# Kernel optimization log

Hardware: AMD Instinct MI355X
Metric: run time of the kernel (lower is better)

## Reference

```python
import jax, jax.numpy as jnp
import numpy as np


def gcn_conv(x, W, src, dst, edge_weight, n_nodes):
    """PyG GCNConv (bias=False, add_self_loops=True, normalize=True).
    out = D^{-1/2} (A + I) D^{-1/2} X W, with deg computed from edge weights
    into each destination node plus the self-loop weight 1.
    """
    h = x @ W  # [N, F_out]
    deg = jax.ops.segment_sum(edge_weight, dst, num_segments=n_nodes) + 1.0  # self-loop w=1
    dinv = jax.lax.rsqrt(deg)  # deg >= 1 so safe
    norm = dinv[src] * edge_weight * dinv[dst]  # [E]
    # gather -> weight -> scatter-add
    agg = jax.ops.segment_sum(norm[:, None] * h[src], dst, num_segments=n_nodes)
    # self-loop contribution: norm_ii = deg_i^{-1}
    return agg + h * (1.0 / deg)[:, None]


def setup_inputs() -> dict:
    key = jax.random.key(0)
    k1, k2, k3, k4, k5 = jax.random.split(key, 5)
    N, E = 10000, 160000
    in_ch, hidden, out_ch = 512, 512, 256
    x = jax.random.normal(k1, (N, in_ch), dtype=jnp.float32)
    edge_index = jax.random.randint(k2, (2, E), 0, N, dtype=jnp.int64)
    edge_weight = jax.random.uniform(k3, (E,), dtype=jnp.float32)
    # Glorot-style init like torch_geometric.nn.dense.linear
    W1 = jax.random.normal(k4, (in_ch, hidden), dtype=jnp.float32) * (1.0 / np.sqrt(in_ch))
    W2 = jax.random.normal(k5, (hidden, out_ch), dtype=jnp.float32) * (1.0 / np.sqrt(hidden))
    return {"x": x, "edge_index": edge_index, "edge_weight": edge_weight, "W1": W1, "W2": W2}


def reference(x, edge_index, edge_weight, W1, W2):
    n_nodes = x.shape[0]
    src, dst = edge_index[0], edge_index[1]
    h = jax.nn.relu(gcn_conv(x, W1, src, dst, edge_weight, n_nodes))
    # dropout is identity in eval mode
    return gcn_conv(h, W2, src, dst, edge_weight, n_nodes)
```

## Files before the change

### kernel.cpp

```cpp
#include <hip/hip_runtime.h>

#define N_NODES 10000
#define N_EDGES 160000
#define M_PAD   10112
#define MT      79
#define KT      8
#define ELLW    64

typedef short s8v __attribute__((ext_vector_type(8)));
typedef short s4v __attribute__((ext_vector_type(4)));
typedef float f4v __attribute__((ext_vector_type(4)));

__device__ inline short f2bf(float f) {
    unsigned u = __builtin_bit_cast(unsigned, f);
    u += 0x7FFF + ((u >> 16) & 1);
    return (short)(u >> 16);
}
__device__ inline float bf2f(short s) {
    return __builtin_bit_cast(float, ((unsigned)(unsigned short)s) << 16);
}

#define GLD_LDS16(g, l)                                                      \
    __builtin_amdgcn_global_load_lds(                                        \
        (const __attribute__((address_space(1))) unsigned int*)(g),          \
        (__attribute__((address_space(3))) unsigned int*)(l), 16, 0, 0)

__global__ __launch_bounds__(256) void k_prep(const float* __restrict__ x,
                                              const float* __restrict__ W1,
                                              const float* __restrict__ W2,
                                              char* __restrict__ x_bf,
                                              char* __restrict__ w1T,
                                              char* __restrict__ w2T,
                                              float* __restrict__ deg,
                                              int* __restrict__ count) {
    int bid = blockIdx.x;
    if (bid < 2528) {
        long long t = (long long)bid * 256 + threadIdx.x;
        int gr = (int)(t >> 6);
        int c  = (int)(t & 63);
        s8v v;
        if (gr < N_NODES) {
            const float* p = &x[(long long)gr * 512 + c * 8];
#pragma unroll
            for (int j = 0; j < 8; j++) v[j] = f2bf(p[j]);
        } else {
#pragma unroll
            for (int j = 0; j < 8; j++) v[j] = 0;
        }
        int r = gr & 127, tm = gr >> 7, tk = c >> 3, sc = c & 7;
        int slot = sc ^ (r & 7);
        *(s8v*)&x_bf[(((long long)tm * KT + tk) << 14) + r * 128 + slot * 16] = v;
    } else if (bid < 2720) {
        const float* W;
        char* out;
        int ncols, t;
        if (bid < 2656) { W = W1; out = w1T; ncols = 512; t = (bid - 2528) * 256 + threadIdx.x; }
        else            { W = W2; out = w2T; ncols = 256; t = (bid - 2656) * 256 + threadIdx.x; }
        int n = t >> 6;
        int c = t & 63;
        s8v v;
#pragma unroll
        for (int j = 0; j < 8; j++) v[j] = f2bf(W[(long long)(c * 8 + j) * ncols + n]);
        int r = n & 127, tn = n >> 7, tk = c >> 3, sc = c & 7;
        int slot = sc ^ (r & 7);
        *(s8v*)&out[(((long long)tn * KT + tk) << 14) + r * 128 + slot * 16] = v;
    } else {
        int i = (bid - 2720) * 256 + threadIdx.x;
        if (i < N_NODES) { deg[i] = 1.0f; count[i] = 0; }
    }
}

__device__ __forceinline__ void gemm_block(const char* __restrict__ ga,
                                           const char* __restrict__ gb,
                                           short* __restrict__ Cb,
                                           int M, int N, int row_blk, int col_blk,
                                           char* As, char* Bs) {
    int tid = threadIdx.x, lane = tid & 63, w = tid >> 6;
    int wr = w >> 1, wc = w & 1;

    f4v acc[4][4];
#pragma unroll
    for (int m = 0; m < 4; m++)
#pragma unroll
        for (int n = 0; n < 4; n++) acc[m][n] = (f4v){0.f, 0.f, 0.f, 0.f};

    for (int kt = 0; kt < KT; ++kt) {
        const char* a0 = ga + (kt << 14);
        const char* b0 = gb + (kt << 14);
#pragma unroll
        for (int j = 0; j < 4; ++j) {
            int off = (j * 256 + w * 64) * 16;
            GLD_LDS16(a0 + off + lane * 16, As + off);
            GLD_LDS16(b0 + off + lane * 16, Bs + off);
        }
        __syncthreads();

#pragma unroll
        for (int kk = 0; kk < 2; ++kk) {
            s8v a[4], b[4];
#pragma unroll
            for (int m = 0; m < 4; ++m) {
                int r = wr * 64 + m * 16 + (lane & 15);
                int slot = ((lane >> 4) + kk * 4) ^ (r & 7);
                a[m] = *(const s8v*)&As[r * 128 + slot * 16];
            }
#pragma unroll
            for (int n = 0; n < 4; ++n) {
                int r = wc * 64 + n * 16 + (lane & 15);
                int slot = ((lane >> 4) + kk * 4) ^ (r & 7);
                b[n] = *(const s8v*)&Bs[r * 128 + slot * 16];
            }
#pragma unroll
            for (int m = 0; m < 4; ++m)
#pragma unroll
                for (int n = 0; n < 4; ++n)
                    acc[m][n] = __builtin_amdgcn_mfma_f32_16x16x32_bf16(a[m], b[n], acc[m][n], 0, 0, 0);
        }
        __syncthreads();
    }

    int row0 = row_blk * 128 + wr * 64;
    int col0 = col_blk * 128 + wc * 64;
#pragma unroll
    for (int m = 0; m < 4; ++m) {
#pragma unroll
        for (int q = 0; q < 4; ++q) {
            int row = row0 + m * 16 + (lane >> 4) * 4 + q;
            if (row < M) {
#pragma unroll
                for (int n = 0; n < 4; ++n) {
                    int col = col0 + n * 16 + (lane & 15);
                    Cb[(long long)row * N + col] = f2bf(acc[m][n][q]);
                }
            }
        }
    }
}

__global__ __launch_bounds__(256) void k_gemm1_deg(const char* __restrict__ A,
                                                   const char* __restrict__ B,
                                                   short* __restrict__ Cb,
                                                   const int* __restrict__ src,
                                                   const int* __restrict__ dst,
                                                   const float* __restrict__ wgt,
                                                   float* __restrict__ deg,
                                                   int* __restrict__ count,
                                                   int2* __restrict__ ell) {
    int bid = blockIdx.x;
    if (bid >= 316) {
        int e = (bid - 316) * 256 + threadIdx.x;
        if (e < N_EDGES) {
            int d = dst[e];
            float wv = wgt[e];
            atomicAdd(&deg[d], wv);
            int pos = atomicAdd(&count[d], 1);
            if (pos < ELLW)
                ell[(long long)d * ELLW + pos] = make_int2(src[e], __float_as_int(wv));
        }
        return;
    }
    __shared__ char As[16384];
    __shared__ char Bs[16384];
    int bx = bid & 3, by = bid >> 2;
    gemm_block(A + ((long long)by * KT << 14), B + ((long long)bx * KT << 14),
               Cb, N_NODES, 512, by, bx, As, Bs);
}

__device__ __forceinline__ void xcd_map(int b, int& by, int& bx) {
    by = (b & 7) * 10 + ((b >> 3) >> 2);
    bx = (b >> 3) & 3;
}

__global__ __launch_bounds__(256) void k_gemm2(const char* __restrict__ A,
                                               const char* __restrict__ w2T,
                                               short* __restrict__ Cb) {
    int by, bx;
    xcd_map(blockIdx.x, by, bx);
    if (by >= MT) return;

    __shared__ char As[16384];
    __shared__ char Bs[8192];
    int tid = threadIdx.x, lane = tid & 63, w = tid >> 6;
    int wr = w >> 1, wc = w & 1;

    const char* ga = A + ((long long)by * KT << 14);
    const char* gbase = w2T + ((long long)(bx >> 1) * KT << 14) + (bx & 1) * 8192;

    f4v acc[4][2];
#pragma unroll
    for (int m = 0; m < 4; m++)
#pragma unroll
        for (int n = 0; n < 2; n++) acc[m][n] = (f4v){0.f, 0.f, 0.f, 0.f};

    for (int kt = 0; kt < KT; ++kt) {
        const char* a0 = ga + (kt << 14);
        const char* b0 = gbase + (kt << 14);
#pragma unroll
        for (int j = 0; j < 4; ++j) {
            int off = (j * 256 + w * 64) * 16;
            GLD_LDS16(a0 + off + lane * 16, As + off);
        }
#pragma unroll
        for (int j = 0; j < 2; ++j) {
            int off = (j * 256 + w * 64) * 16;
            GLD_LDS16(b0 + off + lane * 16, Bs + off);
        }
        __syncthreads();

#pragma unroll
        for (int kk = 0; kk < 2; ++kk) {
            s8v a[4], b[2];
#pragma unroll
            for (int m = 0; m < 4; ++m) {
                int r = wr * 64 + m * 16 + (lane & 15);
                int slot = ((lane >> 4) + kk * 4) ^ (r & 7);
                a[m] = *(const s8v*)&As[r * 128 + slot * 16];
            }
#pragma unroll
            for (int n = 0; n < 2; ++n) {
                int r = wc * 32 + n * 16 + (lane & 15);
                int slot = ((lane >> 4) + kk * 4) ^ (r & 7);
                b[n] = *(const s8v*)&Bs[r * 128 + slot * 16];
            }
#pragma unroll
            for (int m = 0; m < 4; ++m)
#pragma unroll
                for (int n = 0; n < 2; ++n)
                    acc[m][n] = __builtin_amdgcn_mfma_f32_16x16x32_bf16(a[m], b[n], acc[m][n], 0, 0, 0);
        }
        __syncthreads();
    }

    int row0 = by * 128 + wr * 64;
    int col0 = bx * 64 + wc * 32;
#pragma unroll
    for (int m = 0; m < 4; ++m) {
#pragma unroll
        for (int q = 0; q < 4; ++q) {
            int row = row0 + m * 16 + (lane >> 4) * 4 + q;
            if (row < N_NODES) {
#pragma unroll
                for (int n = 0; n < 2; ++n) {
                    int col = col0 + n * 16 + (lane & 15);
                    Cb[(long long)row * 256 + col] = f2bf(acc[m][n][q]);
                }
            }
        }
    }
}

template <int F, bool RELU, bool OUT_TILED>
__global__ __launch_bounds__(256) void k_gather(const int2* __restrict__ ell,
                                                const int* __restrict__ count,
                                                const short* __restrict__ hb,
                                                const float* __restrict__ deg,
                                                void* __restrict__ outp,
                                                int n_waves) {
    const int FPT = F / 64;
    int wave = (int)((blockIdx.x * (long long)blockDim.x + threadIdx.x) >> 6);
    if (wave >= n_waves) return;
    int lane = threadIdx.x & 63;

    float acc[FPT];
#pragma unroll
    for (int j = 0; j < FPT; j++) acc[j] = 0.f;

    if (wave < N_NODES) {
        float dg = deg[wave];
        float inv = 1.0f / dg;
        float dinv_d = rsqrtf(dg);
        {
            if constexpr (FPT == 8) {
                s8v v = *(const s8v*)&hb[(long long)wave * F + lane * 8];
#pragma unroll
                for (int j = 0; j < 8; j++) acc[j] = bf2f(v[j]) * inv;
            } else {
                s4v v = *(const s4v*)&hb[(long long)wave * F + lane * 4];
#pragma unroll
                for (int j = 0; j < 4; j++) acc[j] = bf2f(v[j]) * inv;
            }
        }
        int cnt = count[wave];
        if (cnt > ELLW) cnt = ELLW;
        const int2* row = &ell[(long long)wave * ELLW];
        int p = 0;
        for (; p + 7 < cnt; p += 8) {
            int2 e[8];
#pragma unroll
            for (int q = 0; q < 8; q++) e[q] = row[p + q];
            float nn[8];
#pragma unroll
            for (int q = 0; q < 8; q++)
                nn[q] = rsqrtf(deg[e[q].x]) * __int_as_float(e[q].y) * dinv_d;
            if constexpr (FPT == 8) {
                s8v v[8];
#pragma unroll
                for (int q = 0; q < 8; q++)
                    v[q] = *(const s8v*)&hb[(long long)e[q].x * F + lane * 8];
#pragma unroll
                for (int j = 0; j < 8; j++) {
#pragma unroll
                    for (int q = 0; q < 8; q++) acc[j] += nn[q] * bf2f(v[q][j]);
                }
            } else {
                s4v v[8];
#pragma unroll
                for (int q = 0; q < 8; q++)
                    v[q] = *(const s4v*)&hb[(long long)e[q].x * F + lane * 4];
#pragma unroll
                for (int j = 0; j < 4; j++) {
#pragma unroll
                    for (int q = 0; q < 8; q++) acc[j] += nn[q] * bf2f(v[q][j]);
                }
            }
        }
        for (; p + 3 < cnt; p += 4) {
            int2 e0 = row[p], e1 = row[p + 1], e2 = row[p + 2], e3 = row[p + 3];
            float n0 = rsqrtf(deg[e0.x]) * __int_as_float(e0.y) * dinv_d;
            float n1 = rsqrtf(deg[e1.x]) * __int_as_float(e1.y) * dinv_d;
            float n2 = rsqrtf(deg[e2.x]) * __int_as_float(e2.y) * dinv_d;
            float n3 = rsqrtf(deg[e3.x]) * __int_as_float(e3.y) * dinv_d;
            if constexpr (FPT == 8) {
                s8v v0 = *(const s8v*)&hb[(long long)e0.x * F + lane * 8];
                s8v v1 = *(const s8v*)&hb[(long long)e1.x * F + lane * 8];
                s8v v2 = *(const s8v*)&hb[(long long)e2.x * F + lane * 8];
                s8v v3 = *(const s8v*)&hb[(long long)e3.x * F + lane * 8];
#pragma unroll
                for (int j = 0; j < 8; j++)
                    acc[j] += n0 * bf2f(v0[j]) + n1 * bf2f(v1[j]) + n2 * bf2f(v2[j]) + n3 * bf2f(v3[j]);
            } else {
                s4v v0 = *(const s4v*)&hb[(long long)e0.x * F + lane * 4];
                s4v v1 = *(const s4v*)&hb[(long long)e1.x * F + lane * 4];
                s4v v2 = *(const s4v*)&hb[(long long)e2.x * F + lane * 4];
                s4v v3 = *(const s4v*)&hb[(long long)e3.x * F + lane * 4];
#pragma unroll
                for (int j = 0; j < 4; j++)
                    acc[j] += n0 * bf2f(v0[j]) + n1 * bf2f(v1[j]) + n2 * bf2f(v2[j]) + n3 * bf2f(v3[j]);
            }
        }
        for (; p < cnt; ++p) {
            int2 e0 = row[p];
            float n0 = rsqrtf(deg[e0.x]) * __int_as_float(e0.y) * dinv_d;
            if constexpr (FPT == 8) {
                s8v v0 = *(const s8v*)&hb[(long long)e0.x * F + lane * 8];
#pragma unroll
                for (int j = 0; j < 8; j++) acc[j] += n0 * bf2f(v0[j]);
            } else {
                s4v v0 = *(const s4v*)&hb[(long long)e0.x * F + lane * 4];
#pragma unroll
                for (int j = 0; j < 4; j++) acc[j] += n0 * bf2f(v0[j]);
            }
        }
        if (RELU) {
#pragma unroll
            for (int j = 0; j < FPT; j++) acc[j] = fmaxf(acc[j], 0.f);
        }
    }

    if constexpr (OUT_TILED) {
        s8v v;
#pragma unroll
        for (int j = 0; j < 8; j++) v[j] = f2bf(acc[j]);
        int tm = wave >> 7, r = wave & 127, tk = lane >> 3, sc = lane & 7;
        int slot = sc ^ (r & 7);
        char* out = (char*)outp;
        *(s8v*)&out[(((long long)tm * KT + tk) << 14) + r * 128 + slot * 16] = v;
    } else {
        float* out = (float*)outp + (long long)wave * F + lane * FPT;
#pragma unroll
        for (int j = 0; j < FPT; j += 4) {
            *(float4*)&out[j] = make_float4(acc[j], acc[j + 1], acc[j + 2], acc[j + 3]);
        }
    }
}

extern "C" void kernel_launch(void* const* d_in, const int* in_sizes, int n_in,
                              void* d_out, int out_size, void* d_ws, size_t ws_size,
                              hipStream_t stream) {
    const float* x  = (const float*)d_in[0];
    const int*   ei = (const int*)d_in[1];
    const float* w  = (const float*)d_in[2];
    const float* W1 = (const float*)d_in[3];
    const float* W2 = (const float*)d_in[4];
    float* out = (float*)d_out;

    const int* src = ei;
    const int* dst = ei + N_EDGES;

    char* p = (char*)d_ws;
    auto alloc = [&](size_t bytes) {
        char* r = p;
        p += (bytes + 255) & ~(size_t)255;
        return r;
    };
    char*  x_bf   = alloc((size_t)MT * KT * 16384);
    char*  a1_bf  = alloc((size_t)MT * KT * 16384);
    char*  w1T    = alloc((size_t)4 * KT * 16384);
    char*  w2T    = alloc((size_t)2 * KT * 16384);
    short* h1_bf  = (short*)alloc((size_t)N_NODES * 512 * 2);
    short* h2_bf  = (short*)alloc((size_t)N_NODES * 256 * 2);
    float* deg    = (float*)alloc(N_NODES * 4);
    int*   count  = (int*)alloc(N_NODES * 4);
    int2*  ell    = (int2*)alloc((size_t)N_NODES * ELLW * 8);

    const int B = 256;

    k_prep<<<2760, B, 0, stream>>>(x, W1, W2, x_bf, w1T, w2T, deg, count);
    k_gemm1_deg<<<316 + 625, B, 0, stream>>>(x_bf, w1T, h1_bf, src, dst, w, deg, count, ell);
    k_gather<512, true, true><<<(M_PAD * 64) / B, B, 0, stream>>>(
        ell, count, h1_bf, deg, a1_bf, M_PAD);
    k_gemm2<<<320, B, 0, stream>>>(a1_bf, w2T, h2_bf);
    k_gather<256, false, false><<<(N_NODES * 64) / B, B, 0, stream>>>(
        ell, count, h2_bf, deg, out, N_NODES);
}
```

Baseline: 88.31 us.

## Fuse all five stages into one persistent cooperative kernel with grid syncs

Replaces the five separate kernel launches (prep, gemm1+degree/ELL build, gather1, gemm2, gather2) with a single cooperative kernel. The kernel loops over virtual blocks in each stage and separates stages with grid-wide syncs, capped at 512 resident blocks. This removes per-launch overhead and inter-kernel gaps, but each stage now runs with fewer concurrent blocks than before. It also drops the XCD-aware block mapping for gemm2, and grid syncs add their own cost.

```diff
diff --git a/kernel.cpp b/kernel.cpp
--- a/kernel.cpp
+++ b/kernel.cpp
@@ -1,4 +1,7 @@
 #include <hip/hip_runtime.h>
+#include <hip/hip_cooperative_groups.h>
+
+namespace cg = cooperative_groups;
 
 #define N_NODES 10000
 #define N_EDGES 160000
@@ -25,17 +28,17 @@
         (const __attribute__((address_space(1))) unsigned int*)(g),          \
         (__attribute__((address_space(3))) unsigned int*)(l), 16, 0, 0)
 
-__global__ __launch_bounds__(256) void k_prep(const float* __restrict__ x,
-                                              const float* __restrict__ W1,
-                                              const float* __restrict__ W2,
-                                              char* __restrict__ x_bf,
-                                              char* __restrict__ w1T,
-                                              char* __restrict__ w2T,
-                                              float* __restrict__ deg,
-                                              int* __restrict__ count) {
-    int bid = blockIdx.x;
-    if (bid < 2528) {
-        long long t = (long long)bid * 256 + threadIdx.x;
+__device__ __forceinline__ void prep_unit(int vb, int tid,
+                                          const float* __restrict__ x,
+                                          const float* __restrict__ W1,
+                                          const float* __restrict__ W2,
+                                          char* __restrict__ x_bf,
+                                          char* __restrict__ w1T,
+                                          char* __restrict__ w2T,
+                                          float* __restrict__ deg,
+                                          int* __restrict__ count) {
+    if (vb < 2528) {
+        long long t = (long long)vb * 256 + tid;
         int gr = (int)(t >> 6);
         int c  = (int)(t & 63);
         s8v v;
@@ -50,12 +53,12 @@
         int r = gr & 127, tm = gr >> 7, tk = c >> 3, sc = c & 7;
         int slot = sc ^ (r & 7);
         *(s8v*)&x_bf[(((long long)tm * KT + tk) << 14) + r * 128 + slot * 16] = v;
-    } else if (bid < 2720) {
+    } else if (vb < 2720) {
         const float* W;
         char* out;
         int ncols, t;
-        if (bid < 2656) { W = W1; out = w1T; ncols = 512; t = (bid - 2528) * 256 + threadIdx.x; }
-        else            { W = W2; out = w2T; ncols = 256; t = (bid - 2656) * 256 + threadIdx.x; }
+        if (vb < 2656) { W = W1; out = w1T; ncols = 512; t = (vb - 2528) * 256 + tid; }
+        else           { W = W2; out = w2T; ncols = 256; t = (vb - 2656) * 256 + tid; }
         int n = t >> 6;
         int c = t & 63;
         s8v v;
@@ -65,7 +68,7 @@
         int slot = sc ^ (r & 7);
         *(s8v*)&out[(((long long)tn * KT + tk) << 14) + r * 128 + slot * 16] = v;
     } else {
-        int i = (bid - 2720) * 256 + threadIdx.x;
+        int i = (vb - 2720) * 256 + tid;
         if (i < N_NODES) { deg[i] = 1.0f; count[i] = 0; }
     }
 }
@@ -137,49 +140,12 @@
     }
 }
 
-__global__ __launch_bounds__(256) void k_gemm1_deg(const char* __restrict__ A,
-                                                   const char* __restrict__ B,
-                                                   short* __restrict__ Cb,
-                                                   const int* __restrict__ src,
-                                                   const int* __restrict__ dst,
-                                                   const float* __restrict__ wgt,
-                                                   float* __restrict__ deg,
-                                                   int* __restrict__ count,
-                                                   int2* __restrict__ ell) {
-    int bid = blockIdx.x;
-    if (bid >= 316) {
-        int e = (bid - 316) * 256 + threadIdx.x;
-        if (e < N_EDGES) {
-            int d = dst[e];
-            float wv = wgt[e];
-            atomicAdd(&deg[d], wv);
-            int pos = atomicAdd(&count[d], 1);
-            if (pos < ELLW)
-                ell[(long long)d * ELLW + pos] = make_int2(src[e], __float_as_int(wv));
-        }
-        return;
-    }
-    __shared__ char As[16384];
-    __shared__ char Bs[16384];
-    int bx = bid & 3, by = bid >> 2;
-    gemm_block(A + ((long long)by * KT << 14), B + ((long long)bx * KT << 14),
-               Cb, N_NODES, 512, by, bx, As, Bs);
-}
-
-__device__ __forceinline__ void xcd_map(int b, int& by, int& bx) {
-    by = (b & 7) * 10 + ((b >> 3) >> 2);
-    bx = (b >> 3) & 3;
-}
-
-__global__ __launch_bounds__(256) void k_gemm2(const char* __restrict__ A,
-                                               const char* __restrict__ w2T,
-                                               short* __restrict__ Cb) {
-    int by, bx;
-    xcd_map(blockIdx.x, by, bx);
-    if (by >= MT) return;
-
-    __shared__ char As[16384];
-    __shared__ char Bs[8192];
+__device__ __forceinline__ void gemm2_unit(int vb,
+                                           const char* __restrict__ A,
+                                           const char* __restrict__ w2T,
+                                           short* __restrict__ Cb,
+                                           char* As, char* Bs) {
+    int by = vb >> 2, bx = vb & 3;
     int tid = threadIdx.x, lane = tid & 63, w = tid >> 6;
     int wr = w >> 1, wc = w & 1;
 
@@ -250,39 +216,35 @@
 }
 
 template <int F, bool RELU, bool OUT_TILED>
-__global__ __launch_bounds__(256) void k_gather(const int2* __restrict__ ell,
-                                                const int* __restrict__ count,
-                                                const short* __restrict__ hb,
-                                                const float* __restrict__ deg,
-                                                void* __restrict__ outp,
-                                                int n_waves) {
+__device__ __forceinline__ void gather_unit(int node, int lane,
+                                            const int2* __restrict__ ell,
+                                            const int* __restrict__ count,
+                                            const short* __restrict__ hb,
+                                            const float* __restrict__ deg,
+                                            void* __restrict__ outp) {
     const int FPT = F / 64;
-    int wave = (int)((blockIdx.x * (long long)blockDim.x + threadIdx.x) >> 6);
-    if (wave >= n_waves) return;
-    int lane = threadIdx.x & 63;
-
     float acc[FPT];
 #pragma unroll
     for (int j = 0; j < FPT; j++) acc[j] = 0.f;
 
-    if (wave < N_NODES) {
-        float dg = deg[wave];
+    if (node < N_NODES) {
+        float dg = deg[node];
         float inv = 1.0f / dg;
         float dinv_d = rsqrtf(dg);
         {
             if constexpr (FPT == 8) {
-                s8v v = *(const s8v*)&hb[(long long)wave * F + lane * 8];
+                s8v v = *(const s8v*)&hb[(long long)node * F + lane * 8];
 #pragma unroll
                 for (int j = 0; j < 8; j++) acc[j] = bf2f(v[j]) * inv;
             } else {
-                s4v v = *(const s4v*)&hb[(long long)wave * F + lane * 4];
+                s4v v = *(const s4v*)&hb[(long long)node * F + lane * 4];
 #pragma unroll
                 for (int j = 0; j < 4; j++) acc[j] = bf2f(v[j]) * inv;
             }
         }
-        int cnt = count[wave];
+        int cnt = count[node];
         if (cnt > ELLW) cnt = ELLW;
-        const int2* row = &ell[(long long)wave * ELLW];
+        const int2* row = &ell[(long long)node * ELLW];
         int p = 0;
         for (; p + 7 < cnt; p += 8) {
             int2 e[8];
@@ -361,17 +323,68 @@
         s8v v;
 #pragma unroll
         for (int j = 0; j < 8; j++) v[j] = f2bf(acc[j]);
-        int tm = wave >> 7, r = wave & 127, tk = lane >> 3, sc = lane & 7;
+        int tm = node >> 7, r = node & 127, tk = lane >> 3, sc = lane & 7;
         int slot = sc ^ (r & 7);
         char* out = (char*)outp;
         *(s8v*)&out[(((long long)tm * KT + tk) << 14) + r * 128 + slot * 16] = v;
     } else {
-        float* out = (float*)outp + (long long)wave * F + lane * FPT;
+        float* out = (float*)outp + (long long)node * F + lane * FPT;
 #pragma unroll
         for (int j = 0; j < FPT; j += 4) {
             *(float4*)&out[j] = make_float4(acc[j], acc[j + 1], acc[j + 2], acc[j + 3]);
         }
     }
+}
+
+__global__ __launch_bounds__(256, 2) void k_fused(
+        const float* __restrict__ x, const float* __restrict__ W1,
+        const float* __restrict__ W2, const int* __restrict__ src,
+        const int* __restrict__ dst, const float* __restrict__ wgt,
+        char* __restrict__ x_bf, char* __restrict__ w1T,
+        char* __restrict__ w2T, char* __restrict__ a1_bf,
+        short* __restrict__ h1_bf, short* __restrict__ h2_bf,
+        float* __restrict__ deg, int* __restrict__ count,
+        int2* __restrict__ ell, float* __restrict__ out) {
+    cg::grid_group g = cg::this_grid();
+    __shared__ char As[16384];
+    __shared__ char Bs[16384];
+    int tid = threadIdx.x, lane = tid & 63, wid = tid >> 6;
+    int nb = gridDim.x;
+
+    for (int vb = blockIdx.x; vb < 2760; vb += nb)
+        prep_unit(vb, tid, x, W1, W2, x_bf, w1T, w2T, deg, count);
+    g.sync();
+
+    for (int vb = blockIdx.x; vb < 941; vb += nb) {
+        if (vb < 316) {
+            int bx = vb & 3, by = vb >> 2;
+            gemm_block(x_bf + ((long long)by * KT << 14),
+                       w1T + ((long long)bx * KT << 14),
+                       h1_bf, N_NODES, 512, by, bx, As, Bs);
+        } else {
+            int e = (vb - 316) * 256 + tid;
+            if (e < N_EDGES) {
+                int d = dst[e];
+                float wv = wgt[e];
+                atomicAdd(&deg[d], wv);
+                int pos = atomicAdd(&count[d], 1);
+                if (pos < ELLW)
+                    ell[(long long)d * ELLW + pos] = make_int2(src[e], __float_as_int(wv));
+            }
+        }
+    }
+    g.sync();
+
+    for (int node = (blockIdx.x << 2) | wid; node < M_PAD; node += nb * 4)
+        gather_unit<512, true, true>(node, lane, ell, count, h1_bf, deg, a1_bf);
+    g.sync();
+
+    for (int vb = blockIdx.x; vb < 320; vb += nb)
+        gemm2_unit(vb, a1_bf, w2T, h2_bf, As, Bs);
+    g.sync();
+
+    for (int node = (blockIdx.x << 2) | wid; node < N_NODES; node += nb * 4)
+        gather_unit<256, false, false>(node, lane, ell, count, h2_bf, deg, out);
 }
 
 extern "C" void kernel_launch(void* const* d_in, const int* in_sizes, int n_in,
@@ -403,13 +416,20 @@
     int*   count  = (int*)alloc(N_NODES * 4);
     int2*  ell    = (int2*)alloc((size_t)N_NODES * ELLW * 8);
 
-    const int B = 256;
-
-    k_prep<<<2760, B, 0, stream>>>(x, W1, W2, x_bf, w1T, w2T, deg, count);
-    k_gemm1_deg<<<316 + 625, B, 0, stream>>>(x_bf, w1T, h1_bf, src, dst, w, deg, count, ell);
-    k_gather<512, true, true><<<(M_PAD * 64) / B, B, 0, stream>>>(
-        ell, count, h1_bf, deg, a1_bf, M_PAD);
-    k_gemm2<<<320, B, 0, stream>>>(a1_bf, w2T, h2_bf);
-    k_gather<256, false, false><<<(N_NODES * 64) / B, B, 0, stream>>>(
-        ell, count, h2_bf, deg, out, N_NODES);
-}
+    int blocks_per_cu = 0;
+    if (hipOccupancyMaxActiveBlocksPerMultiprocessor(
+            &blocks_per_cu, (const void*)k_fused, 256, 0) != hipSuccess ||
+        blocks_per_cu < 1)
+        blocks_per_cu = 1;
+    int grid = blocks_per_cu * 256;
+    if (grid > 512) grid = 512;
+
+    void* args[] = {
+        (void*)&x, (void*)&W1, (void*)&W2, (void*)&src, (void*)&dst, (void*)&w,
+        (void*)&x_bf, (void*)&w1T, (void*)&w2T, (void*)&a1_bf,
+        (void*)&h1_bf, (void*)&h2_bf, (void*)&deg, (void*)&count,
+        (void*)&ell, (void*)&out
+    };
+    (void)hipLaunchCooperativeKernel((const void*)k_fused, dim3(grid), dim3(256),
+                                     args, 0, stream);
+}
```

Result: slower. 268.5 us (+204.1%).

## Split layer-1 gather into two half-feature waves per node and XCD-map GEMM1 blocks

Applied to the files above, without the earlier changes.

The first aggregation now assigns two waves per node, each handling 256 of the 512 features with 8-byte loads, which doubles the wave count to raise memory-level parallelism in the gather. Each half-wave writes its 8-byte piece into the swizzled tiled layout that GEMM2 reads. GEMM1 blocks are now remapped with the XCD-aware mapping already used by GEMM2, padding the grid to 320 tiles, to improve L2 locality across chiplets. The trade-off is that edge lists and degree values are read twice per node in the first gather.

```diff
diff --git a/kernel.cpp b/kernel.cpp
--- a/kernel.cpp
+++ b/kernel.cpp
@@ -70,6 +70,11 @@
     }
 }
 
+__device__ __forceinline__ void xcd_map(int b, int& by, int& bx) {
+    by = (b & 7) * 10 + ((b >> 3) >> 2);
+    bx = (b >> 3) & 3;
+}
+
 __device__ __forceinline__ void gemm_block(const char* __restrict__ ga,
                                            const char* __restrict__ gb,
                                            short* __restrict__ Cb,
@@ -147,8 +152,8 @@
                                                    int* __restrict__ count,
                                                    int2* __restrict__ ell) {
     int bid = blockIdx.x;
-    if (bid >= 316) {
-        int e = (bid - 316) * 256 + threadIdx.x;
+    if (bid >= 320) {
+        int e = (bid - 320) * 256 + threadIdx.x;
         if (e < N_EDGES) {
             int d = dst[e];
             float wv = wgt[e];
@@ -159,16 +164,13 @@
         }
         return;
     }
+    int by, bx;
+    xcd_map(bid, by, bx);
+    if (by >= MT) return;
     __shared__ char As[16384];
     __shared__ char Bs[16384];
-    int bx = bid & 3, by = bid >> 2;
     gemm_block(A + ((long long)by * KT << 14), B + ((long long)bx * KT << 14),
                Cb, N_NODES, 512, by, bx, As, Bs);
-}
-
-__device__ __forceinline__ void xcd_map(int b, int& by, int& bx) {
-    by = (b & 7) * 10 + ((b >> 3) >> 2);
-    bx = (b >> 3) & 3;
 }
 
 __global__ __launch_bounds__(256) void k_gemm2(const char* __restrict__ A,
@@ -249,40 +251,31 @@
     }
 }
 
-template <int F, bool RELU, bool OUT_TILED>
-__global__ __launch_bounds__(256) void k_gather(const int2* __restrict__ ell,
-                                                const int* __restrict__ count,
-                                                const short* __restrict__ hb,
-                                                const float* __restrict__ deg,
-                                                void* __restrict__ outp,
-                                                int n_waves) {
-    const int FPT = F / 64;
-    int wave = (int)((blockIdx.x * (long long)blockDim.x + threadIdx.x) >> 6);
-    if (wave >= n_waves) return;
+__global__ __launch_bounds__(256) void k_gather1(const int2* __restrict__ ell,
+                                                 const int* __restrict__ count,
+                                                 const short* __restrict__ hb,
+                                                 const float* __restrict__ deg,
+                                                 char* __restrict__ outp) {
+    int gw = (int)((blockIdx.x * (long long)blockDim.x + threadIdx.x) >> 6);
+    if (gw >= M_PAD * 2) return;
+    int node = gw >> 1, h = gw & 1;
     int lane = threadIdx.x & 63;
-
-    float acc[FPT];
-#pragma unroll
-    for (int j = 0; j < FPT; j++) acc[j] = 0.f;
-
-    if (wave < N_NODES) {
-        float dg = deg[wave];
+    int col0 = h * 256 + lane * 4;
+
+    float acc[4] = {0.f, 0.f, 0.f, 0.f};
+
+    if (node < N_NODES) {
+        float dg = deg[node];
         float inv = 1.0f / dg;
         float dinv_d = rsqrtf(dg);
         {
-            if constexpr (FPT == 8) {
-                s8v v = *(const s8v*)&hb[(long long)wave * F + lane * 8];
-#pragma unroll
-                for (int j = 0; j < 8; j++) acc[j] = bf2f(v[j]) * inv;
-            } else {
-                s4v v = *(const s4v*)&hb[(long long)wave * F + lane * 4];
-#pragma unroll
-                for (int j = 0; j < 4; j++) acc[j] = bf2f(v[j]) * inv;
-            }
-        }
-        int cnt = count[wave];
+            s4v v = *(const s4v*)&hb[(long long)node * 512 + col0];
+#pragma unroll
+            for (int j = 0; j < 4; j++) acc[j] = bf2f(v[j]) * inv;
+        }
+        int cnt = count[node];
         if (cnt > ELLW) cnt = ELLW;
-        const int2* row = &ell[(long long)wave * ELLW];
+        const int2* row = &ell[(long long)node * ELLW];
         int p = 0;
         for (; p + 7 < cnt; p += 8) {
             int2 e[8];
@@ -292,26 +285,14 @@
 #pragma unroll
             for (int q = 0; q < 8; q++)
                 nn[q] = rsqrtf(deg[e[q].x]) * __int_as_float(e[q].y) * dinv_d;
-            if constexpr (FPT == 8) {
-                s8v v[8];
-#pragma unroll
-                for (int q = 0; q < 8; q++)
-                    v[q] = *(const s8v*)&hb[(long long)e[q].x * F + lane * 8];
-#pragma unroll
-                for (int j = 0; j < 8; j++) {
-#pragma unroll
-                    for (int q = 0; q < 8; q++) acc[j] += nn[q] * bf2f(v[q][j]);
-                }
-            } else {
-                s4v v[8];
-#pragma unroll
-                for (int q = 0; q < 8; q++)
-                    v[q] = *(const s4v*)&hb[(long long)e[q].x * F + lane * 4];
-#pragma unroll
-                for (int j = 0; j < 4; j++) {
-#pragma unroll
-                    for (int q = 0; q < 8; q++) acc[j] += nn[q] * bf2f(v[q][j]);
-                }
+            s4v v[8];
+#pragma unroll
+            for (int q = 0; q < 8; q++)
+                v[q] = *(const s4v*)&hb[(long long)e[q].x * 512 + col0];
+#pragma unroll
+            for (int j = 0; j < 4; j++) {
+#pragma unroll
+                for (int q = 0; q < 8; q++) acc[j] += nn[q] * bf2f(v[q][j]);
             }
         }
         for (; p + 3 < cnt; p += 4) {
@@ -320,58 +301,97 @@
             float n1 = rsqrtf(deg[e1.x]) * __int_as_float(e1.y) * dinv_d;
             float n2 = rsqrtf(deg[e2.x]) * __int_as_float(e2.y) * dinv_d;
             float n3 = rsqrtf(deg[e3.x]) * __int_as_float(e3.y) * dinv_d;
-            if constexpr (FPT == 8) {
-                s8v v0 = *(const s8v*)&hb[(long long)e0.x * F + lane * 8];
-                s8v v1 = *(const s8v*)&hb[(long long)e1.x * F + lane * 8];
-                s8v v2 = *(const s8v*)&hb[(long long)e2.x * F + lane * 8];
-                s8v v3 = *(const s8v*)&hb[(long long)e3.x * F + lane * 8];
-#pragma unroll
-                for (int j = 0; j < 8; j++)
-                    acc[j] += n0 * bf2f(v0[j]) + n1 * bf2f(v1[j]) + n2 * bf2f(v2[j]) + n3 * bf2f(v3[j]);
-            } else {
-                s4v v0 = *(const s4v*)&hb[(long long)e0.x * F + lane * 4];
-                s4v v1 = *(const s4v*)&hb[(long long)e1.x * F + lane * 4];
-                s4v v2 = *(const s4v*)&hb[(long long)e2.x * F + lane * 4];
-                s4v v3 = *(const s4v*)&hb[(long long)e3.x * F + lane * 4];
-#pragma unroll
-                for (int j = 0; j < 4; j++)
-                    acc[j] += n0 * bf2f(v0[j]) + n1 * bf2f(v1[j]) + n2 * bf2f(v2[j]) + n3 * bf2f(v3[j]);
-            }
+            s4v v0 = *(const s4v*)&hb[(long long)e0.x * 512 + col0];
+            s4v v1 = *(const s4v*)&hb[(long long)e1.x * 512 + col0];
+            s4v v2 = *(const s4v*)&hb[(long long)e2.x * 512 + col0];
+            s4v v3 = *(const s4v*)&hb[(long long)e3.x * 512 + col0];
+#pragma unroll
+            for (int j = 0; j < 4; j++)
+                acc[j] += n0 * bf2f(v0[j]) + n1 * bf2f(v1[j]) + n2 * bf2f(v2[j]) + n3 * bf2f(v3[j]);
         }
         for (; p < cnt; ++p) {
             int2 e0 = row[p];
             float n0 = rsqrtf(deg[e0.x]) * __int_as_float(e0.y) * dinv_d;
-            if constexpr (FPT == 8) {
-                s8v v0 = *(const s8v*)&hb[(long long)e0.x * F + lane * 8];
-#pragma unroll
-                for (int j = 0; j < 8; j++) acc[j] += n0 * bf2f(v0[j]);
-            } else {
-                s4v v0 = *(const s4v*)&hb[(long long)e0.x * F + lane * 4];
-#pragma unroll
-                for (int j = 0; j < 4; j++) acc[j] += n0 * bf2f(v0[j]);
-            }
-        }
-        if (RELU) {
-#pragma unroll
-            for (int j = 0; j < FPT; j++) acc[j] = fmaxf(acc[j], 0.f);
-        }
-    }
-
-    if constexpr (OUT_TILED) {
-        s8v v;
-#pragma unroll
-        for (int j = 0; j < 8; j++) v[j] = f2bf(acc[j]);
-        int tm = wave >> 7, r = wave & 127, tk = lane >> 3, sc = lane & 7;
-        int slot = sc ^ (r & 7);
-        char* out = (char*)outp;
-        *(s8v*)&out[(((long long)tm * KT + tk) << 14) + r * 128 + slot * 16] = v;
-    } else {
-        float* out = (float*)outp + (long long)wave * F + lane * FPT;
-#pragma unroll
-        for (int j = 0; j < FPT; j += 4) {
-            *(float4*)&out[j] = make_float4(acc[j], acc[j + 1], acc[j + 2], acc[j + 3]);
-        }
-    }
+            s4v v0 = *(const s4v*)&hb[(long long)e0.x * 512 + col0];
+#pragma unroll
+            for (int j = 0; j < 4; j++) acc[j] += n0 * bf2f(v0[j]);
+        }
+#pragma unroll
+        for (int j = 0; j < 4; j++) acc[j] = fmaxf(acc[j], 0.f);
+    }
+
+    s4v o;
+#pragma unroll
+    for (int j = 0; j < 4; j++) o[j] = f2bf(acc[j]);
+    int tm = node >> 7, r = node & 127;
+    int tk = col0 >> 6, sc = (col0 >> 3) & 7;
+    int slot = sc ^ (r & 7);
+    *(s4v*)&outp[(((long long)tm * KT + tk) << 14) + r * 128 + slot * 16 + (lane & 1) * 8] = o;
+}
+
+__global__ __launch_bounds__(256) void k_gather2(const int2* __restrict__ ell,
+                                                 const int* __restrict__ count,
+                                                 const short* __restrict__ hb,
+                                                 const float* __restrict__ deg,
+                                                 float* __restrict__ out) {
+    int node = (int)((blockIdx.x * (long long)blockDim.x + threadIdx.x) >> 6);
+    if (node >= N_NODES) return;
+    int lane = threadIdx.x & 63;
+
+    float acc[4];
+    float dg = deg[node];
+    float inv = 1.0f / dg;
+    float dinv_d = rsqrtf(dg);
+    {
+        s4v v = *(const s4v*)&hb[(long long)node * 256 + lane * 4];
+#pragma unroll
+        for (int j = 0; j < 4; j++) acc[j] = bf2f(v[j]) * inv;
+    }
+    int cnt = count[node];
+    if (cnt > ELLW) cnt = ELLW;
+    const int2* row = &ell[(long long)node * ELLW];
+    int p = 0;
+    for (; p + 7 < cnt; p += 8) {
+        int2 e[8];
+#pragma unroll
+        for (int q = 0; q < 8; q++) e[q] = row[p + q];
+        float nn[8];
+#pragma unroll
+        for (int q = 0; q < 8; q++)
+            nn[q] = rsqrtf(deg[e[q].x]) * __int_as_float(e[q].y) * dinv_d;
+        s4v v[8];
+#pragma unroll
+        for (int q = 0; q < 8; q++)
+            v[q] = *(const s4v*)&hb[(long long)e[q].x * 256 + lane * 4];
+#pragma unroll
+        for (int j = 0; j < 4; j++) {
+#pragma unroll
+            for (int q = 0; q < 8; q++) acc[j] += nn[q] * bf2f(v[q][j]);
+        }
+    }
+    for (; p + 3 < cnt; p += 4) {
+        int2 e0 = row[p], e1 = row[p + 1], e2 = row[p + 2], e3 = row[p + 3];
+        float n0 = rsqrtf(deg[e0.x]) * __int_as_float(e0.y) * dinv_d;
+        float n1 = rsqrtf(deg[e1.x]) * __int_as_float(e1.y) * dinv_d;
+        float n2 = rsqrtf(deg[e2.x]) * __int_as_float(e2.y) * dinv_d;
+        float n3 = rsqrtf(deg[e3.x]) * __int_as_float(e3.y) * dinv_d;
+        s4v v0 = *(const s4v*)&hb[(long long)e0.x * 256 + lane * 4];
+        s4v v1 = *(const s4v*)&hb[(long long)e1.x * 256 + lane * 4];
+        s4v v2 = *(const s4v*)&hb[(long long)e2.x * 256 + lane * 4];
+        s4v v3 = *(const s4v*)&hb[(long long)e3.x * 256 + lane * 4];
+#pragma unroll
+        for (int j = 0; j < 4; j++)
+            acc[j] += n0 * bf2f(v0[j]) + n1 * bf2f(v1[j]) + n2 * bf2f(v2[j]) + n3 * bf2f(v3[j]);
+    }
+    for (; p < cnt; ++p) {
+        int2 e0 = row[p];
+        float n0 = rsqrtf(deg[e0.x]) * __int_as_float(e0.y) * dinv_d;
+        s4v v0 = *(const s4v*)&hb[(long long)e0.x * 256 + lane * 4];
+#pragma unroll
+        for (int j = 0; j < 4; j++) acc[j] += n0 * bf2f(v0[j]);
+    }
+    *(float4*)&out[(long long)node * 256 + lane * 4] =
+        make_float4(acc[0], acc[1], acc[2], acc[3]);
 }
 
 extern "C" void kernel_launch(void* const* d_in, const int* in_sizes, int n_in,
@@ -406,10 +426,8 @@
     const int B = 256;
 
     k_prep<<<2760, B, 0, stream>>>(x, W1, W2, x_bf, w1T, w2T, deg, count);
-    k_gemm1_deg<<<316 + 625, B, 0, stream>>>(x_bf, w1T, h1_bf, src, dst, w, deg, count, ell);
-    k_gather<512, true, true><<<(M_PAD * 64) / B, B, 0, stream>>>(
-        ell, count, h1_bf, deg, a1_bf, M_PAD);
+    k_gemm1_deg<<<320 + 625, B, 0, stream>>>(x_bf, w1T, h1_bf, src, dst, w, deg, count, ell);
+    k_gather1<<<(M_PAD * 2 * 64) / B, B, 0, stream>>>(ell, count, h1_bf, deg, a1_bf);
     k_gemm2<<<320, B, 0, stream>>>(a1_bf, w2T, h2_bf);
-    k_gather<256, false, false><<<(N_NODES * 64) / B, B, 0, stream>>>(
-        ell, count, h2_bf, deg, out, N_NODES);
-}
+    k_gather2<<<(N_NODES * 64) / B, B, 0, stream>>>(ell, count, h2_bf, deg, out);
+}
```

Result: no change. 88.66 us (+0.4%).
